# Performance work log

Measured on AMD Instinct MI355X. Metric: run time of the kernel, lower is better.

## Reference

```python
import jax, jax.numpy as jnp
import numpy as np

NEG_SLOPE = 0.15
MASK_VAL = -1e9


def setup_inputs() -> dict:
    key = jax.random.key(0)
    k1, k2, k3, k4, k5 = jax.random.split(key, 5)
    B, N, D, H, QKV = 4, 1024, 128, 8, 16
    h = jax.random.normal(k1, (B, N, D), dtype=jnp.float32)
    same_cluster = jax.random.randint(k2, (B, N, N), 0, 2) > 0
    # nn.Linear weights stored as [in, out] (x @ W); scaled like default init
    Wa = jax.random.normal(k3, (2 * D + 1, H), dtype=jnp.float32) / np.sqrt(2 * D + 1)
    Wv = jax.random.normal(k4, (D, H * QKV), dtype=jnp.float32) / np.sqrt(D)
    Wo = jax.random.normal(k5, (H * QKV, D), dtype=jnp.float32) / np.sqrt(H * QKV)
    return {"h": h, "same_cluster": same_cluster, "Wa": Wa, "Wv": Wv, "Wo": Wo, "local_only": 0}


def reference(h, same_cluster, Wa, Wv, Wo, local_only):
    B, N, D = h.shape
    H = Wa.shape[1]
    # concat([hi, hj, edge]) @ Wa == hi @ Wa[:D] + hj @ Wa[D:2D] + edge * Wa[2D]
    Wa_i, Wa_j, w_e = Wa[:D], Wa[D:2 * D], Wa[2 * D]  # [D,H], [D,H], [H]
    s_i = h @ Wa_i  # [B, N, H]
    s_j = h @ Wa_j  # [B, N, H]
    edge = same_cluster.astype(h.dtype)  # [B, N, N]
    scores = s_i[:, :, None, :] + s_j[:, None, :, :] + edge[..., None] * w_e  # [B,N,N,H]
    scores = jax.nn.leaky_relu(scores, negative_slope=NEG_SLOPE)
    scores = jnp.moveaxis(scores, -1, 1)  # [B, H, N, N]
    if local_only:
        scores = jnp.where(same_cluster[:, None, :, :], scores, MASK_VAL)
    alpha = jax.nn.softmax(scores, axis=-1)  # [B, H, N, N]
    v = (h @ Wv).reshape(B, N, H, -1).transpose(0, 2, 1, 3)  # [B, H, N, qkv]
    out = jnp.einsum('bhij,bhjd->bhid', alpha, v)  # [B, H, N, qkv]
    out = out.transpose(0, 2, 1, 3).reshape(B, N, -1)  # [B, N, H*qkv]
    return out @ Wo  # [B, N, D]
```

## Files before the change

kernel.cpp:

```cpp
#include <hip/hip_runtime.h>
#include <hip/hip_bf16.h>


#define NEG_SLOPE 0.15f
#define B_ 4
#define N_ 1024
#define D_ 128
#define H_ 8
#define QKV_ 16
#define BN_ (B_ * N_)

__global__ __launch_bounds__(256) void prep_kernel(
    const float* __restrict__ h, const float* __restrict__ Wa,
    const float* __restrict__ Wv, float* __restrict__ SIt,
    float* __restrict__ SJt, float* __restrict__ V)
{
    __shared__ float hl[4][128];
    const int t  = threadIdx.x;
    const int R0 = blockIdx.x * 4;

    if (t < 128) {
        const int r = t >> 5, k = (t & 31) * 4;
        *(float4*)&hl[r][k] = *(const float4*)(h + (R0 + r) * 128 + k);
    }
    __syncthreads();

    const int c = t & 127, g = t >> 7;
    float acc0 = 0.f, acc1 = 0.f;
    #pragma unroll 4
    for (int k = 0; k < 128; ++k) {
        const float wv = Wv[k * 128 + c];
        acc0 += hl[g * 2 + 0][k] * wv;
        acc1 += hl[g * 2 + 1][k] * wv;
    }
    const int head = c >> 4, dd = c & 15;
    {
        int R = R0 + g * 2;
        int b = R >> 10, n = R & 1023;
        V[((b * H_ + head) * N_ + n) * QKV_ + dd] = acc0;
        R += 1; b = R >> 10; n = R & 1023;
        V[((b * H_ + head) * N_ + n) * QKV_ + dd] = acc1;
    }

    {
        const int row = t >> 6, which = (t >> 5) & 1, hh = (t >> 2) & 7, q = t & 3;
        const float* wcol = Wa + which * 128 * H_ + hh;
        float s = 0.f;
        #pragma unroll
        for (int kk = 0; kk < 32; ++kk) {
            const int k = q * 32 + kk;
            s += hl[row][k] * wcol[k * H_];
        }
        s += __shfl_xor(s, 1, 64);
        s += __shfl_xor(s, 2, 64);
        if (q == 0) {
            float* dst = which ? SJt : SIt;
            dst[hh * BN_ + R0 + row] = s;
        }
    }
}

__global__ __launch_bounds__(256) void attn_kernel(
    const float* __restrict__ SIt, const float* __restrict__ SJt,
    const float* __restrict__ V, const int* __restrict__ edge,
    const float* __restrict__ Wa, const int* __restrict__ local_only,
    float* __restrict__ ATT)
{
    const int t  = threadIdx.x;
    const int w  = t >> 6;
    const int l  = t & 63;
    const int hh = blockIdx.y;
    const int b  = blockIdx.z;
    const int i0 = blockIdx.x * 16 + w * 4;
    const int bn0 = b * N_;

    const float we = Wa[2 * D_ * H_ + hh];
    const int   lo = local_only[0];

    float si[4];
    #pragma unroll
    for (int r = 0; r < 4; ++r) si[r] = SIt[hh * BN_ + bn0 + i0 + r];

    const float* vbase  = V + (size_t)(b * H_ + hh) * N_ * QKV_;
    const float* sjbase = SJt + hh * BN_ + bn0;
    const int*   ebase  = edge + (size_t)(bn0 + i0) * N_;

    float acc[4][16];
    #pragma unroll
    for (int r = 0; r < 4; ++r)
        #pragma unroll
        for (int d = 0; d < 16; ++d) acc[r][d] = 0.f;
    float dsum[4] = {0.f, 0.f, 0.f, 0.f};

    for (int j0 = 0; j0 < N_; j0 += 64) {
        const int j = j0 + l;
        const float sj = sjbase[j];
        const float4* vp = (const float4*)(vbase + j * QKV_);
        const float4 v0 = vp[0], v1 = vp[1], v2 = vp[2], v3 = vp[3];
        int e[4];
        #pragma unroll
        for (int r = 0; r < 4; ++r) e[r] = ebase[r * N_ + j];

        #pragma unroll
        for (int r = 0; r < 4; ++r) {
            float sc = si[r] + sj + (e[r] ? we : 0.f);
            sc = fmaxf(sc, NEG_SLOPE * sc);
            float p = __expf(sc);
            if (lo && !e[r]) p = 0.f;
            dsum[r] += p;
            acc[r][0]  += p * v0.x; acc[r][1]  += p * v0.y;
            acc[r][2]  += p * v0.z; acc[r][3]  += p * v0.w;
            acc[r][4]  += p * v1.x; acc[r][5]  += p * v1.y;
            acc[r][6]  += p * v1.z; acc[r][7]  += p * v1.w;
            acc[r][8]  += p * v2.x; acc[r][9]  += p * v2.y;
            acc[r][10] += p * v2.z; acc[r][11] += p * v2.w;
            acc[r][12] += p * v3.x; acc[r][13] += p * v3.y;
            acc[r][14] += p * v3.z; acc[r][15] += p * v3.w;
        }
    }

    #pragma unroll
    for (int r = 0; r < 4; ++r) {
        #pragma unroll
        for (int m = 1; m < 64; m <<= 1) dsum[r] += __shfl_xor(dsum[r], m, 64);
        #pragma unroll
        for (int d = 0; d < 16; ++d) {
            #pragma unroll
            for (int m = 1; m < 64; m <<= 1)
                acc[r][d] += __shfl_xor(acc[r][d], m, 64);
        }
    }

    if (l == 0) {
        #pragma unroll
        for (int r = 0; r < 4; ++r) {
            const float inv = 1.0f / dsum[r];
            float* dst = ATT + (size_t)(bn0 + i0 + r) * 128 + hh * 16;
            #pragma unroll
            for (int q = 0; q < 4; ++q) {
                float4 o;
                o.x = acc[r][4 * q + 0] * inv;
                o.y = acc[r][4 * q + 1] * inv;
                o.z = acc[r][4 * q + 2] * inv;
                o.w = acc[r][4 * q + 3] * inv;
                *(float4*)(dst + 4 * q) = o;
            }
        }
    }
}

__global__ __launch_bounds__(256) void out_kernel(
    const float* __restrict__ ATT, const float* __restrict__ Wo,
    float* __restrict__ out)
{
    __shared__ float al[4][128];
    const int t  = threadIdx.x;
    const int R0 = blockIdx.x * 4;
    if (t < 128) {
        const int r = t >> 5, k = (t & 31) * 4;
        *(float4*)&al[r][k] = *(const float4*)(ATT + (R0 + r) * 128 + k);
    }
    __syncthreads();

    const int c = t & 127, g = t >> 7;
    float acc0 = 0.f, acc1 = 0.f;
    #pragma unroll 4
    for (int k = 0; k < 128; ++k) {
        const float w = Wo[k * 128 + c];
        acc0 += al[g * 2 + 0][k] * w;
        acc1 += al[g * 2 + 1][k] * w;
    }
    out[(R0 + g * 2 + 0) * 128 + c] = acc0;
    out[(R0 + g * 2 + 1) * 128 + c] = acc1;
}

extern "C" void kernel_launch(void* const* d_in, const int* in_sizes, int n_in,
                              void* d_out, int out_size, void* d_ws, size_t ws_size,
                              hipStream_t stream) {
    const float* h    = (const float*)d_in[0];
    const int*   edge = (const int*)d_in[1];
    const float* Wa   = (const float*)d_in[2];
    const float* Wv   = (const float*)d_in[3];
    const float* Wo   = (const float*)d_in[4];
    const int*   lo   = (const int*)d_in[5];
    float*       out  = (float*)d_out;

    float* ws  = (float*)d_ws;
    float* SIt = ws;
    float* SJt = SIt + H_ * BN_;
    float* V   = SJt + H_ * BN_;
    float* ATT = V + (size_t)B_ * H_ * N_ * QKV_;

    prep_kernel<<<BN_ / 4, 256, 0, stream>>>(h, Wa, Wv, SIt, SJt, V);
    attn_kernel<<<dim3(N_ / 16, H_, B_), 256, 0, stream>>>(SIt, SJt, V, edge, Wa, lo, ATT);
    out_kernel<<<BN_ / 4, 256, 0, stream>>>(ATT, Wo, out);
}
```

Measured before the change: 147.6 us.

## Vectorize projection kernels, use transpose-reduce butterfly in attention epilogue

The prep and output projection kernels now handle 8 rows per block, with each thread computing 4 output columns from float4 weight loads, and V is written with float4 stores. The attention epilogue replaces 68 full butterfly reductions per row-group with a recursive-halving transpose-reduce. That leaves each lane holding one output element, so all 64 lanes write ATT in parallel instead of lane 0 writing serially. The attention kernel also gains a launch-bounds occupancy hint and an unroll-2 pragma, which may raise register pressure or cause spills.

```diff
diff --git a/kernel.cpp b/kernel.cpp
--- a/kernel.cpp
+++ b/kernel.cpp
@@ -15,52 +15,51 @@
     const float* __restrict__ Wv, float* __restrict__ SIt,
     float* __restrict__ SJt, float* __restrict__ V)
 {
-    __shared__ float hl[4][128];
+    __shared__ float hl[8][128];
     const int t  = threadIdx.x;
-    const int R0 = blockIdx.x * 4;
-
-    if (t < 128) {
-        const int r = t >> 5, k = (t & 31) * 4;
-        *(float4*)&hl[r][k] = *(const float4*)(h + (R0 + r) * 128 + k);
+    const int R0 = blockIdx.x * 8;
+
+    {
+        const int f = t * 4;
+        *(float4*)(&hl[0][0] + f) = *(const float4*)(h + R0 * 128 + f);
     }
     __syncthreads();
 
-    const int c = t & 127, g = t >> 7;
-    float acc0 = 0.f, acc1 = 0.f;
-    #pragma unroll 4
+    const int cq = t & 31, rq = t >> 5;
+    const int c4 = cq * 4;
+    float acc0 = 0.f, acc1 = 0.f, acc2 = 0.f, acc3 = 0.f;
+    #pragma unroll 8
     for (int k = 0; k < 128; ++k) {
-        const float wv = Wv[k * 128 + c];
-        acc0 += hl[g * 2 + 0][k] * wv;
-        acc1 += hl[g * 2 + 1][k] * wv;
-    }
-    const int head = c >> 4, dd = c & 15;
-    {
-        int R = R0 + g * 2;
-        int b = R >> 10, n = R & 1023;
-        V[((b * H_ + head) * N_ + n) * QKV_ + dd] = acc0;
-        R += 1; b = R >> 10; n = R & 1023;
-        V[((b * H_ + head) * N_ + n) * QKV_ + dd] = acc1;
-    }
-
-    {
-        const int row = t >> 6, which = (t >> 5) & 1, hh = (t >> 2) & 7, q = t & 3;
+        const float4 w = *(const float4*)(Wv + k * 128 + c4);
+        const float a = hl[rq][k];
+        acc0 += a * w.x; acc1 += a * w.y; acc2 += a * w.z; acc3 += a * w.w;
+    }
+    {
+        const int R = R0 + rq, b = R >> 10, n = R & 1023;
+        const int head = cq >> 2, dd = (cq & 3) * 4;
+        float4 o; o.x = acc0; o.y = acc1; o.z = acc2; o.w = acc3;
+        *(float4*)(V + ((size_t)(b * H_ + head) * N_ + n) * QKV_ + dd) = o;
+    }
+
+    {
+        const int task = t >> 1, half = t & 1;
+        const int row = task >> 4, which = (task >> 3) & 1, hh = task & 7;
         const float* wcol = Wa + which * 128 * H_ + hh;
         float s = 0.f;
-        #pragma unroll
-        for (int kk = 0; kk < 32; ++kk) {
-            const int k = q * 32 + kk;
+        #pragma unroll 8
+        for (int kk = 0; kk < 64; ++kk) {
+            const int k = half * 64 + kk;
             s += hl[row][k] * wcol[k * H_];
         }
         s += __shfl_xor(s, 1, 64);
-        s += __shfl_xor(s, 2, 64);
-        if (q == 0) {
+        if (!half) {
             float* dst = which ? SJt : SIt;
             dst[hh * BN_ + R0 + row] = s;
         }
     }
 }
 
-__global__ __launch_bounds__(256) void attn_kernel(
+__global__ __launch_bounds__(256, 4) void attn_kernel(
     const float* __restrict__ SIt, const float* __restrict__ SJt,
     const float* __restrict__ V, const int* __restrict__ edge,
     const float* __restrict__ Wa, const int* __restrict__ local_only,
@@ -92,6 +91,7 @@
         for (int d = 0; d < 16; ++d) acc[r][d] = 0.f;
     float dsum[4] = {0.f, 0.f, 0.f, 0.f};
 
+    #pragma unroll 2
     for (int j0 = 0; j0 < N_; j0 += 64) {
         const int j = j0 + l;
         const float sj = sjbase[j];
@@ -119,33 +119,57 @@
         }
     }
 
+    const bool b3 = (l & 8) != 0;
+    const bool b2 = (l & 4) != 0;
+    const bool b1 = (l & 2) != 0;
+    const bool b0 = (l & 1) != 0;
+    float red[4];
     #pragma unroll
     for (int r = 0; r < 4; ++r) {
-        #pragma unroll
-        for (int m = 1; m < 64; m <<= 1) dsum[r] += __shfl_xor(dsum[r], m, 64);
-        #pragma unroll
-        for (int d = 0; d < 16; ++d) {
-            #pragma unroll
-            for (int m = 1; m < 64; m <<= 1)
-                acc[r][d] += __shfl_xor(acc[r][d], m, 64);
-        }
-    }
-
-    if (l == 0) {
-        #pragma unroll
-        for (int r = 0; r < 4; ++r) {
-            const float inv = 1.0f / dsum[r];
-            float* dst = ATT + (size_t)(bn0 + i0 + r) * 128 + hh * 16;
-            #pragma unroll
-            for (int q = 0; q < 4; ++q) {
-                float4 o;
-                o.x = acc[r][4 * q + 0] * inv;
-                o.y = acc[r][4 * q + 1] * inv;
-                o.z = acc[r][4 * q + 2] * inv;
-                o.w = acc[r][4 * q + 3] * inv;
-                *(float4*)(dst + 4 * q) = o;
-            }
-        }
+        float ds = dsum[r];
+        #pragma unroll
+        for (int m = 1; m < 64; m <<= 1) ds += __shfl_xor(ds, m, 64);
+        dsum[r] = ds;
+
+        float t8[8];
+        #pragma unroll
+        for (int d = 0; d < 8; ++d) {
+            const float keep = b3 ? acc[r][d + 8] : acc[r][d];
+            const float send = b3 ? acc[r][d]     : acc[r][d + 8];
+            t8[d] = keep + __shfl_xor(send, 8, 64);
+        }
+        float t4[4];
+        #pragma unroll
+        for (int d = 0; d < 4; ++d) {
+            const float keep = b2 ? t8[d + 4] : t8[d];
+            const float send = b2 ? t8[d]     : t8[d + 4];
+            t4[d] = keep + __shfl_xor(send, 4, 64);
+        }
+        float t2[2];
+        #pragma unroll
+        for (int d = 0; d < 2; ++d) {
+            const float keep = b1 ? t4[d + 2] : t4[d];
+            const float send = b1 ? t4[d]     : t4[d + 2];
+            t2[d] = keep + __shfl_xor(send, 2, 64);
+        }
+        float t1;
+        {
+            const float keep = b0 ? t2[1] : t2[0];
+            const float send = b0 ? t2[0] : t2[1];
+            t1 = keep + __shfl_xor(send, 1, 64);
+        }
+        t1 += __shfl_xor(t1, 16, 64);
+        t1 += __shfl_xor(t1, 32, 64);
+        red[r] = t1;
+    }
+
+    {
+        const int rsel = l >> 4;
+        const float num = rsel == 0 ? red[0] : rsel == 1 ? red[1]
+                        : rsel == 2 ? red[2] : red[3];
+        const float den = rsel == 0 ? dsum[0] : rsel == 1 ? dsum[1]
+                        : rsel == 2 ? dsum[2] : dsum[3];
+        ATT[(size_t)(bn0 + i0 + rsel) * 128 + hh * 16 + (l & 15)] = num / den;
     }
 }
 
@@ -153,25 +177,26 @@
     const float* __restrict__ ATT, const float* __restrict__ Wo,
     float* __restrict__ out)
 {
-    __shared__ float al[4][128];
+    __shared__ float al[8][128];
     const int t  = threadIdx.x;
-    const int R0 = blockIdx.x * 4;
-    if (t < 128) {
-        const int r = t >> 5, k = (t & 31) * 4;
-        *(float4*)&al[r][k] = *(const float4*)(ATT + (R0 + r) * 128 + k);
+    const int R0 = blockIdx.x * 8;
+    {
+        const int f = t * 4;
+        *(float4*)(&al[0][0] + f) = *(const float4*)(ATT + (size_t)R0 * 128 + f);
     }
     __syncthreads();
 
-    const int c = t & 127, g = t >> 7;
-    float acc0 = 0.f, acc1 = 0.f;
-    #pragma unroll 4
+    const int cq = t & 31, rq = t >> 5;
+    const int c4 = cq * 4;
+    float acc0 = 0.f, acc1 = 0.f, acc2 = 0.f, acc3 = 0.f;
+    #pragma unroll 8
     for (int k = 0; k < 128; ++k) {
-        const float w = Wo[k * 128 + c];
-        acc0 += al[g * 2 + 0][k] * w;
-        acc1 += al[g * 2 + 1][k] * w;
-    }
-    out[(R0 + g * 2 + 0) * 128 + c] = acc0;
-    out[(R0 + g * 2 + 1) * 128 + c] = acc1;
+        const float4 w = *(const float4*)(Wo + k * 128 + c4);
+        const float a = al[rq][k];
+        acc0 += a * w.x; acc1 += a * w.y; acc2 += a * w.z; acc3 += a * w.w;
+    }
+    float4 o; o.x = acc0; o.y = acc1; o.z = acc2; o.w = acc3;
+    *(float4*)(out + (size_t)(R0 + rq) * 128 + c4) = o;
 }
 
 extern "C" void kernel_launch(void* const* d_in, const int* in_sizes, int n_in,
@@ -191,7 +216,7 @@
     float* V   = SJt + H_ * BN_;
     float* ATT = V + (size_t)B_ * H_ * N_ * QKV_;
 
-    prep_kernel<<<BN_ / 4, 256, 0, stream>>>(h, Wa, Wv, SIt, SJt, V);
+    prep_kernel<<<BN_ / 8, 256, 0, stream>>>(h, Wa, Wv, SIt, SJt, V);
     attn_kernel<<<dim3(N_ / 16, H_, B_), 256, 0, stream>>>(SIt, SJt, V, edge, Wa, lo, ATT);
-    out_kernel<<<BN_ / 4, 256, 0, stream>>>(ATT, Wo, out);
-}
+    out_kernel<<<BN_ / 8, 256, 0, stream>>>(ATT, Wo, out);
+}
```

New measurement: 133.1 us. 1.11x faster.
